# Kernel optimization log

Measured on AMD Instinct MI355X. Metric: run time of the kernel, lower is better.

The kernel has to match this reference:

```python
import jax, jax.numpy as jnp
import numpy as np

NUM_CLASSES = 80
RESO = 416
ANCHORS = np.array([[116.0, 90.0], [156.0, 198.0], [373.0, 326.0]], dtype=np.float32)  # (nA, 2)


def setup_inputs() -> dict:
    key = jax.random.key(0)
    bs, gs = 512, 13
    nA = ANCHORS.shape[0]
    num_attrs = 5 + NUM_CLASSES
    x = jax.random.normal(key, (bs, nA * num_attrs, gs, gs), dtype=jnp.float32)
    return {"x": x}


def reference(x):
    # YOLO detection-head decode (inference path of YOLOLayer.forward)
    bs, _, gs, _ = x.shape
    stride = RESO // gs
    nA = ANCHORS.shape[0]
    num_attrs = 5 + NUM_CLASSES
    scaled_anchors = jnp.asarray(ANCHORS) / jnp.float32(stride)  # (nA, 2)

    # (bs, nA, num_attrs, gs, gs) -> (bs, nA, gs, gs, num_attrs)
    xr = x.reshape(bs, nA, num_attrs, gs, gs).transpose(0, 1, 3, 4, 2)

    pred_tx = jax.nn.sigmoid(xr[..., 0])
    pred_ty = jax.nn.sigmoid(xr[..., 1])
    pred_tw = xr[..., 2]
    pred_th = xr[..., 3]
    pred_conf = jax.nn.sigmoid(xr[..., 4])
    pred_cls = jax.nn.softmax(xr[..., 5:], axis=-1)

    grid = jnp.arange(gs, dtype=jnp.float32)
    grid_x = grid[None, None, None, :]  # varies along last grid axis (i)
    grid_y = grid[None, None, :, None]  # varies along row axis (j)
    anchor_w = scaled_anchors[:, 0][None, :, None, None]
    anchor_h = scaled_anchors[:, 1][None, :, None, None]

    s = jnp.float32(stride)
    bx = (pred_tx + grid_x) * s
    by = (pred_ty + grid_y) * s
    bw = jnp.exp(pred_tw) * anchor_w * s
    bh = jnp.exp(pred_th) * anchor_h * s

    pred = jnp.concatenate(
        [bx[..., None], by[..., None], bw[..., None], bh[..., None],
         pred_conf[..., None], pred_cls],
        axis=-1,
    )  # (bs, nA, gs, gs, num_attrs)
    return pred.reshape(bs, -1, num_attrs)
```

## Files before the change

### kernel.cpp

```cpp
#include <hip/hip_runtime.h>
#include <math.h>

namespace {

constexpr int kNA      = 3;
constexpr int kGS      = 13;
constexpr int kAttrs   = 85;
constexpr int kSpatial = kGS * kGS;
constexpr int kCells   = 512 * kNA * kSpatial;
constexpr float kStrideF = 32.0f;

constexpr int kBlockThreads  = 256;
constexpr int kThreadsPerCell = 4;
constexpr int kCellsPerBlock = kBlockThreads / kThreadsPerCell;
constexpr int kSmemFloats    = kCellsPerBlock * kAttrs;
constexpr int kSmemFloat4    = kSmemFloats / 4;
constexpr int kMaxAttrsPerThread = 22;

__device__ __forceinline__ float fsigmoid(float x) {
    return 1.0f / (1.0f + __expf(-x));
}

__global__ __launch_bounds__(kBlockThreads) void yolo_head_kernel(const float* __restrict__ x,
                                                                  float* __restrict__ out) {
    __shared__ float smem[kSmemFloats];

    const int tid  = threadIdx.x;
    const int q    = tid & 3;
    const int cl   = tid >> 2;
    const int cell = blockIdx.x * kCellsPerBlock + cl;

    const int s  = cell % kSpatial;
    const int ba = cell / kSpatial;
    const int a  = ba % kNA;

    const float* __restrict__ xp = x + (size_t)ba * kAttrs * kSpatial + s;

    float v[kMaxAttrsPerThread];
#pragma unroll
    for (int i = 0; i < kMaxAttrsPerThread; ++i) {
        const int c = q + 4 * i;
        if (c < kAttrs) v[i] = xp[(size_t)c * kSpatial];
    }

    float m = -INFINITY;
#pragma unroll
    for (int i = 0; i < kMaxAttrsPerThread; ++i) {
        const int c = q + 4 * i;
        if (c >= 5 && c < kAttrs) m = fmaxf(m, v[i]);
    }
    m = fmaxf(m, __shfl_xor(m, 1, 64));
    m = fmaxf(m, __shfl_xor(m, 2, 64));

    float sum = 0.0f;
#pragma unroll
    for (int i = 0; i < kMaxAttrsPerThread; ++i) {
        const int c = q + 4 * i;
        if (c >= 5 && c < kAttrs) {
            v[i] = __expf(v[i] - m);
            sum += v[i];
        }
    }
    sum += __shfl_xor(sum, 1, 64);
    sum += __shfl_xor(sum, 2, 64);
    const float inv = 1.0f / sum;

    float* __restrict__ sp = smem + cl * kAttrs;

    if (q == 0) {
        const float jf = (float)(s % kGS);
        sp[0] = (fsigmoid(v[0]) + jf) * kStrideF;
        sp[4] = fsigmoid(v[1]);
    } else if (q == 1) {
        const float if_ = (float)(s / kGS);
        sp[1] = (fsigmoid(v[0]) + if_) * kStrideF;
    } else if (q == 2) {
        const float aw = (a == 0) ? 116.0f : (a == 1) ? 156.0f : 373.0f;
        sp[2] = __expf(v[0]) * aw;
    } else {
        const float ah = (a == 0) ? 90.0f : (a == 1) ? 198.0f : 326.0f;
        sp[3] = __expf(v[0]) * ah;
    }
#pragma unroll
    for (int i = 0; i < kMaxAttrsPerThread; ++i) {
        const int c = q + 4 * i;
        if (c >= 5 && c < kAttrs) sp[c] = v[i] * inv;
    }

    __syncthreads();

    const float4* __restrict__ s4 = (const float4*)smem;
    float4* __restrict__ out4 = (float4*)(out + (size_t)blockIdx.x * kSmemFloats);
#pragma unroll 2
    for (int t = tid; t < kSmemFloat4; t += kBlockThreads) {
        out4[t] = s4[t];
    }
}

}

extern "C" void kernel_launch(void* const* d_in, const int* in_sizes, int n_in,
                              void* d_out, int out_size, void* d_ws, size_t ws_size,
                              hipStream_t stream) {
    const float* x = (const float*)d_in[0];
    float* out = (float*)d_out;
    const int blocks = kCells / kCellsPerBlock;
    yolo_head_kernel<<<blocks, kBlockThreads, 0, stream>>>(x, out);
}
```

Before: 39.83 us.

## Stage whole per-anchor slab in LDS with vectorized loads before decode

Each block now owns one (batch, anchor) slab: it copies the full 85x169 input slab into LDS using float4 global loads, then decodes cells in three passes and writes each output chunk back with float4 stores. This replaces the strided scalar global reads (stride of 169 floats per attribute) with contiguous vectorized reads. In exchange it uses about 79 KB of LDS per block, which lowers occupancy, and adds serialized passes with extra barriers.

```diff
diff --git a/kernel.cpp b/kernel.cpp
--- a/kernel.cpp
+++ b/kernel.cpp
@@ -7,93 +7,124 @@
 constexpr int kGS      = 13;
 constexpr int kAttrs   = 85;
 constexpr int kSpatial = kGS * kGS;
-constexpr int kCells   = 512 * kNA * kSpatial;
+constexpr int kSlabs   = 512 * kNA;
+constexpr int kSlab    = kAttrs * kSpatial;
 constexpr float kStrideF = 32.0f;
 
-constexpr int kBlockThreads  = 256;
-constexpr int kThreadsPerCell = 4;
-constexpr int kCellsPerBlock = kBlockThreads / kThreadsPerCell;
-constexpr int kSmemFloats    = kCellsPerBlock * kAttrs;
-constexpr int kSmemFloat4    = kSmemFloats / 4;
-constexpr int kMaxAttrsPerThread = 22;
+constexpr int kBlockThreads = 256;
+constexpr int kCellsPerPass = 64;
+constexpr int kChunkFloats  = kCellsPerPass * kAttrs;
+constexpr int kAttrsPerLane = 22;
 
 __device__ __forceinline__ float fsigmoid(float x) {
     return 1.0f / (1.0f + __expf(-x));
 }
 
-__global__ __launch_bounds__(kBlockThreads) void yolo_head_kernel(const float* __restrict__ x,
+
+__device__ __forceinline__ void load_slab_to_lds(const float* __restrict__ src,
+                                                 float* __restrict__ lds, int n, int tid) {
+    const int lead = (int)((16u - ((uintptr_t)src & 15u)) & 15u) >> 2;
+    if (tid < lead) lds[tid] = src[tid];
+    const int nv = (n - lead) >> 2;
+    const float4* __restrict__ s4 = (const float4*)(src + lead);
+    for (int t = tid; t < nv; t += kBlockThreads) {
+        const float4 d = s4[t];
+        const int o = lead + (t << 2);
+        lds[o] = d.x; lds[o + 1] = d.y; lds[o + 2] = d.z; lds[o + 3] = d.w;
+    }
+    const int done = lead + (nv << 2);
+    if (tid < n - done) lds[done + tid] = src[done + tid];
+}
+
+__device__ __forceinline__ void store_lds_to_global(float* __restrict__ dst,
+                                                    const float* __restrict__ lds, int n, int tid) {
+    const int lead = (int)((16u - ((uintptr_t)dst & 15u)) & 15u) >> 2;
+    if (tid < lead) dst[tid] = lds[tid];
+    const int nv = (n - lead) >> 2;
+    float4* __restrict__ d4 = (float4*)(dst + lead);
+    for (int t = tid; t < nv; t += kBlockThreads) {
+        const int o = lead + (t << 2);
+        float4 d;
+        d.x = lds[o]; d.y = lds[o + 1]; d.z = lds[o + 2]; d.w = lds[o + 3];
+        d4[t] = d;
+    }
+    const int done = lead + (nv << 2);
+    if (tid < n - done) dst[done + tid] = lds[done + tid];
+}
+
+__global__ __launch_bounds__(kBlockThreads) void yolo_slab_kernel(const float* __restrict__ x,
                                                                   float* __restrict__ out) {
-    __shared__ float smem[kSmemFloats];
+    __shared__ float in_s[kSlab + 3];
+    __shared__ float out_s[kChunkFloats];
 
-    const int tid  = threadIdx.x;
-    const int q    = tid & 3;
-    const int cl   = tid >> 2;
-    const int cell = blockIdx.x * kCellsPerBlock + cl;
+    const int tid = threadIdx.x;
+    const int ba  = blockIdx.x;
+    const int a   = ba % kNA;
+    const size_t base = (size_t)ba * kSlab;
 
-    const int s  = cell % kSpatial;
-    const int ba = cell / kSpatial;
-    const int a  = ba % kNA;
-
-    const float* __restrict__ xp = x + (size_t)ba * kAttrs * kSpatial + s;
-
-    float v[kMaxAttrsPerThread];
-#pragma unroll
-    for (int i = 0; i < kMaxAttrsPerThread; ++i) {
-        const int c = q + 4 * i;
-        if (c < kAttrs) v[i] = xp[(size_t)c * kSpatial];
-    }
-
-    float m = -INFINITY;
-#pragma unroll
-    for (int i = 0; i < kMaxAttrsPerThread; ++i) {
-        const int c = q + 4 * i;
-        if (c >= 5 && c < kAttrs) m = fmaxf(m, v[i]);
-    }
-    m = fmaxf(m, __shfl_xor(m, 1, 64));
-    m = fmaxf(m, __shfl_xor(m, 2, 64));
-
-    float sum = 0.0f;
-#pragma unroll
-    for (int i = 0; i < kMaxAttrsPerThread; ++i) {
-        const int c = q + 4 * i;
-        if (c >= 5 && c < kAttrs) {
-            v[i] = __expf(v[i] - m);
-            sum += v[i];
-        }
-    }
-    sum += __shfl_xor(sum, 1, 64);
-    sum += __shfl_xor(sum, 2, 64);
-    const float inv = 1.0f / sum;
-
-    float* __restrict__ sp = smem + cl * kAttrs;
-
-    if (q == 0) {
-        const float jf = (float)(s % kGS);
-        sp[0] = (fsigmoid(v[0]) + jf) * kStrideF;
-        sp[4] = fsigmoid(v[1]);
-    } else if (q == 1) {
-        const float if_ = (float)(s / kGS);
-        sp[1] = (fsigmoid(v[0]) + if_) * kStrideF;
-    } else if (q == 2) {
-        const float aw = (a == 0) ? 116.0f : (a == 1) ? 156.0f : 373.0f;
-        sp[2] = __expf(v[0]) * aw;
-    } else {
-        const float ah = (a == 0) ? 90.0f : (a == 1) ? 198.0f : 326.0f;
-        sp[3] = __expf(v[0]) * ah;
-    }
-#pragma unroll
-    for (int i = 0; i < kMaxAttrsPerThread; ++i) {
-        const int c = q + 4 * i;
-        if (c >= 5 && c < kAttrs) sp[c] = v[i] * inv;
-    }
-
+    load_slab_to_lds(x + base, in_s, kSlab, tid);
     __syncthreads();
 
-    const float4* __restrict__ s4 = (const float4*)smem;
-    float4* __restrict__ out4 = (float4*)(out + (size_t)blockIdx.x * kSmemFloats);
-#pragma unroll 2
-    for (int t = tid; t < kSmemFloat4; t += kBlockThreads) {
-        out4[t] = s4[t];
+    const int q  = tid & 3;
+    const int cl = tid >> 2;
+
+    const float aw = (a == 0) ? 116.0f : (a == 1) ? 156.0f : 373.0f;
+    const float ah = (a == 0) ?  90.0f : (a == 1) ? 198.0f : 326.0f;
+
+    for (int p = 0; p < 3; ++p) {
+        const int s = p * kCellsPerPass + cl;
+        if (s < kSpatial) {
+            float v[kAttrsPerLane];
+#pragma unroll
+            for (int i = 0; i < kAttrsPerLane; ++i) {
+                const int c = q + 4 * i;
+                if (c < kAttrs) v[i] = in_s[c * kSpatial + s];
+            }
+
+            float m = -INFINITY;
+#pragma unroll
+            for (int i = 0; i < kAttrsPerLane; ++i) {
+                const int c = q + 4 * i;
+                if (c >= 5 && c < kAttrs) m = fmaxf(m, v[i]);
+            }
+            m = fmaxf(m, __shfl_xor(m, 1, 64));
+            m = fmaxf(m, __shfl_xor(m, 2, 64));
+
+            float sum = 0.0f;
+#pragma unroll
+            for (int i = 0; i < kAttrsPerLane; ++i) {
+                const int c = q + 4 * i;
+                if (c >= 5 && c < kAttrs) {
+                    v[i] = __expf(v[i] - m);
+                    sum += v[i];
+                }
+            }
+            sum += __shfl_xor(sum, 1, 64);
+            sum += __shfl_xor(sum, 2, 64);
+            const float inv = 1.0f / sum;
+
+            float* __restrict__ sp = out_s + cl * kAttrs;
+            if (q == 0) {
+                sp[0] = (fsigmoid(v[0]) + (float)(s % kGS)) * kStrideF;
+                sp[4] = fsigmoid(v[1]);
+            } else if (q == 1) {
+                sp[1] = (fsigmoid(v[0]) + (float)(s / kGS)) * kStrideF;
+            } else if (q == 2) {
+                sp[2] = __expf(v[0]) * aw;
+            } else {
+                sp[3] = __expf(v[0]) * ah;
+            }
+#pragma unroll
+            for (int i = 0; i < kAttrsPerLane; ++i) {
+                const int c = q + 4 * i;
+                if (c >= 5 && c < kAttrs) sp[c] = v[i] * inv;
+            }
+        }
+        __syncthreads();
+
+        const int ncells = (p == 2) ? (kSpatial - 2 * kCellsPerPass) : kCellsPerPass;
+        store_lds_to_global(out + base + (size_t)p * kChunkFloats, out_s, ncells * kAttrs, tid);
+        __syncthreads();
     }
 }
 
@@ -104,6 +135,5 @@
                               hipStream_t stream) {
     const float* x = (const float*)d_in[0];
     float* out = (float*)d_out;
-    const int blocks = kCells / kCellsPerBlock;
-    yolo_head_kernel<<<blocks, kBlockThreads, 0, stream>>>(x, out);
+    yolo_slab_kernel<<<kSlabs, kBlockThreads, 0, stream>>>(x, out);
 }
```

Measured after the change: 44.27 us. +11.2%, slower.
